# Performance work log

Hardware: AMD Instinct MI355X
Metric: run time of the kernel (lower is better)

## Reference

```python
import jax, jax.numpy as jnp
import numpy as np
from jax import lax

N, C, H, W = 64, 96, 18, 32
S_IN = 320          # input_state_size
HEADS, HD = 4, 96 // 4
HID = 96            # HIDDEN_SIZE
ENC = 320           # ENC_SIZE
K = 3               # KERNEL_SIZE


def _conv(x, k, b):
    y = lax.conv_general_dilated(x, k, (1, 1), 'SAME',
                                 dimension_numbers=('NCHW', 'OIHW', 'NCHW'))
    return y + b[None, :, None, None]


def setup_inputs() -> dict:
    key = jax.random.key(0)
    ks = jax.random.split(key, 16)
    sc = 0.02
    inp = {
        'x': jax.random.normal(ks[0], (N, C, H, W), jnp.float32),
        'x_state': jax.random.normal(ks[1], (N, S_IN), jnp.float32),
        'actor_keys': jax.random.randint(ks[2], (N,), 0, N),
        'hidden_states': 0.1 * jax.random.normal(ks[3], (N, HID, H, W), jnp.float32),
        # modulation Linear(S_IN -> 2*C), bias init 0
        'W_mod': sc * jax.random.normal(ks[4], (S_IN, 2 * C), jnp.float32),
        'b_mod': jnp.zeros((2 * C,), jnp.float32),
        # FiLM attention: qkv 1x1 proj and output proj
        'W_qkv': sc * jax.random.normal(ks[5], (C, 3 * C), jnp.float32),
        'b_qkv': jnp.zeros((3 * C,), jnp.float32),
        'W_proj': sc * jax.random.normal(ks[6], (C, C), jnp.float32),
        'b_proj': jnp.zeros((C,), jnp.float32),
        # IRConv2dCell (ConvGRU-style): gates conv (2C -> 2*HID), candidate conv (2C -> HID)
        'K_zr': sc * jax.random.normal(ks[7], (2 * HID, 2 * C, K, K), jnp.float32),
        'b_zr': jnp.zeros((2 * HID,), jnp.float32),
        'K_c': sc * jax.random.normal(ks[8], (HID, 2 * C, K, K), jnp.float32),
        'b_c': jnp.zeros((HID,), jnp.float32),
        # PosConv: learned positional map + 1x1 conv to ENC
        'pos_emb': sc * jax.random.normal(ks[9], (1, HID, H, W), jnp.float32),
        'W_pos': sc * jax.random.normal(ks[10], (ENC, HID), jnp.float32),
        'b_pos': jnp.zeros((ENC,), jnp.float32),
    }
    return inp


def reference(x, x_state, actor_keys, hidden_states,
              W_mod, b_mod, W_qkv, b_qkv, W_proj, b_proj,
              K_zr, b_zr, K_c, b_c, pos_emb, W_pos, b_pos):
    HW = H * W
    # modulation -> FiLM params
    mod = x_state @ W_mod + b_mod                       # [N, 2C]
    mm, mb = jnp.split(mod, 2, axis=1)                  # [N, C] each
    # FiLM-conditioned attention over spatial positions
    xm = x * mm[:, :, None, None] + mb[:, :, None, None]  # [N,C,H,W]
    xf = xm.reshape(N, C, HW).transpose(0, 2, 1)          # [N,HW,C]
    qkv = xf @ W_qkv + b_qkv                              # [N,HW,3C]
    q, k, v = jnp.split(qkv, 3, axis=-1)
    q = q.reshape(N, HW, HEADS, HD).transpose(0, 2, 1, 3)  # [N,h,HW,hd]
    k = k.reshape(N, HW, HEADS, HD).transpose(0, 2, 1, 3)
    v = v.reshape(N, HW, HEADS, HD).transpose(0, 2, 1, 3)
    attn = jax.nn.softmax(jnp.einsum('nhqd,nhkd->nhqk', q, k) / np.sqrt(HD), axis=-1)
    o = jnp.einsum('nhqk,nhkd->nhqd', attn, v)            # [N,h,HW,hd]
    o = o.transpose(0, 2, 1, 3).reshape(N, HW, C)
    o = o @ W_proj + b_proj
    y = x + o.transpose(0, 2, 1).reshape(N, C, H, W)      # residual
    # actor-keyed recurrent conv memory cell (gather per actor key)
    h = hidden_states[actor_keys]                         # [N,HID,H,W]
    xh = jnp.concatenate([y, h], axis=1)                  # [N,2C,H,W]
    zr = _conv(xh, K_zr, b_zr)
    z, r = jnp.split(jax.nn.sigmoid(zr), 2, axis=1)
    c = jnp.tanh(_conv(jnp.concatenate([y, r * h], axis=1), K_c, b_c))
    h_new = (1.0 - z) * h + z * c                         # [N,HID,H,W]
    # pooled outputs
    x_visual = h_new.reshape(N, HID, H // 2, 2, W // 2, 2).mean(axis=(3, 5))
    e = h_new + pos_emb
    enc = jnp.einsum('nchw,oc->nohw', e, W_pos) + b_pos[None, :, None, None]
    x_visual_enc = enc.max(axis=(2, 3))                   # [N,ENC]
    return (x_visual, x_visual_enc)
```

## Files before the change

kernel.cpp:

```cpp
#include <hip/hip_runtime.h>
#include <hip/hip_bf16.h>
#include <math.h>

#define NN 64
#define CC 96
#define HH 18
#define WW 32
#define HWP 576
#define SIN 320
#define NHEADS 4
#define HDIM 24
#define HIDC 96
#define ENCC 320

#define MOD_OFF   0
#define A_OFF     12288
#define Y_OFF     (A_OFF)
#define Z_OFF     (A_OFF + 3538944)
#define RH_OFF    (A_OFF + 7077888)
#define O_OFF     (A_OFF + 10616832)
#define HN_OFF    (O_OFF)
#define PART_OFF  (O_OFF + 3538944)
#define WTZR_OFF  (PART_OFF + 163840)
#define WTC_OFF   (WTZR_OFF + 165888)

typedef __attribute__((ext_vector_type(8))) short short8;
typedef __attribute__((ext_vector_type(4))) float f32x4;
typedef __attribute__((ext_vector_type(2))) unsigned int uint2v;
#define MFMA16(a, b, c) __builtin_amdgcn_mfma_f32_16x16x32_bf16(a, b, c, 0, 0, 0)

__device__ inline unsigned short f2bf(float f) {
  __hip_bfloat16 h = __float2bfloat16(f);
  return *reinterpret_cast<unsigned short*>(&h);
}
__device__ inline unsigned int cvtpk(float lo, float hi) {
  unsigned int r;
  asm volatile("v_cvt_pk_bf16_f32 %0, %1, %2" : "=v"(r) : "v"(lo), "v"(hi));
  return r;
}
union S8U { short8 s; unsigned int u[4]; };

__global__ __launch_bounds__(192) void k_mod(const float* __restrict__ xs,
    const float* __restrict__ Wm, const float* __restrict__ bm,
    float* __restrict__ mod) {
  __shared__ float s[SIN];
  int n = blockIdx.x;
  for (int i = threadIdx.x; i < SIN; i += 192) s[i] = xs[n * SIN + i];
  __syncthreads();
  int j = threadIdx.x;
  float acc = bm[j];
  #pragma unroll 4
  for (int k = 0; k < SIN; ++k) acc = fmaf(s[k], Wm[k * 192 + j], acc);
  mod[n * 192 + j] = acc;
}

__global__ __launch_bounds__(256) void k_qkv(const float* __restrict__ x,
    const float* __restrict__ mod, const float* __restrict__ Wq,
    const float* __restrict__ bq, float* __restrict__ qkv) {
  int id = blockIdx.x;
  int n = id & 63, pt = id >> 6;
  int p0 = pt * 96;
  __shared__ __align__(16) short XT[96 * 104];
  int tid = threadIdx.x, lane = tid & 63, wid = tid >> 6;
  int wr = wid >> 1, wcn = wid & 1;
  int cl = lane & 15, kg = lane >> 4;
  #pragma unroll
  for (int w = 0; w < 9; ++w) {
    int lin = tid + 256 * w;
    int cp = lin / 48, pp = (lin % 48) * 2;
    float mA = mod[n * 192 + 2 * cp], bA = mod[n * 192 + 96 + 2 * cp];
    float mB = mod[n * 192 + 2 * cp + 1], bB = mod[n * 192 + 96 + 2 * cp + 1];
    float2 xa = *reinterpret_cast<const float2*>(
        &x[((size_t)n * CC + 2 * cp) * HWP + p0 + pp]);
    float2 xb = *reinterpret_cast<const float2*>(
        &x[((size_t)n * CC + 2 * cp + 1) * HWP + p0 + pp]);
    *reinterpret_cast<unsigned int*>(&XT[pp * 104 + 2 * cp]) =
        cvtpk(fmaf(xa.x, mA, bA), fmaf(xb.x, mB, bB));
    *reinterpret_cast<unsigned int*>(&XT[(pp + 1) * 104 + 2 * cp]) =
        cvtpk(fmaf(xa.y, mA, bA), fmaf(xb.y, mB, bB));
  }
  __syncthreads();

  f32x4 acc[3][9];
  #pragma unroll
  for (int mt = 0; mt < 3; ++mt)
    #pragma unroll
    for (int nt = 0; nt < 9; ++nt) acc[mt][nt] = (f32x4){0.f, 0.f, 0.f, 0.f};

  #pragma unroll
  for (int kc = 0; kc < 3; ++kc) {
    short8 af[3];
    #pragma unroll
    for (int mt = 0; mt < 3; ++mt) {
      int row = wr * 48 + mt * 16 + cl;
      af[mt] = *reinterpret_cast<const short8*>(
          &XT[row * 104 + kc * 32 + kg * 8]);
    }
    #pragma unroll
    for (int nt = 0; nt < 9; ++nt) {
      int j = wcn * 144 + nt * 16 + cl;
      const float* wp = Wq + (size_t)(kc * 32 + kg * 8) * 288 + j;
      S8U b;
      b.u[0] = cvtpk(wp[0], wp[288]);
      b.u[1] = cvtpk(wp[576], wp[864]);
      b.u[2] = cvtpk(wp[1152], wp[1440]);
      b.u[3] = cvtpk(wp[1728], wp[2016]);
      #pragma unroll
      for (int mt = 0; mt < 3; ++mt)
        acc[mt][nt] = MFMA16(af[mt], b.s, acc[mt][nt]);
    }
  }

  #pragma unroll
  for (int nt = 0; nt < 9; ++nt) {
    int j = wcn * 144 + nt * 16 + cl;
    float bias = bq[j];
    #pragma unroll
    for (int mt = 0; mt < 3; ++mt) {
      int pr = p0 + wr * 48 + mt * 16 + kg * 4;
      float* dst = qkv + ((size_t)n * HWP + pr) * 288 + j;
      dst[0] = acc[mt][nt][0] + bias;
      dst[288] = acc[mt][nt][1] + bias;
      dst[576] = acc[mt][nt][2] + bias;
      dst[864] = acc[mt][nt][3] + bias;
    }
  }
}

__global__ __launch_bounds__(256) void k_attn(const float* __restrict__ qkv,
                                              float* __restrict__ o) {
  int id = blockIdx.x;
  int n = id & 63, head = id >> 6;
  __shared__ __align__(16) short K_lds[576 * 40];
  __shared__ __align__(16) short VT_lds[24 * 584];
  __shared__ __align__(16) short P_lds[4 * 144 * 40];
  int tid = threadIdx.x, lane = tid & 63, wid = tid >> 6;
  int cl = lane & 15, kg = lane >> 4;
  const float* base = qkv + (size_t)n * HWP * 288;
  int qoff = head * HDIM, koff = CC + head * HDIM, voff = 2 * CC + head * HDIM;
  const float scale = 0.2041241452319315f;

  for (int p = tid; p < HWP; p += 256) {
    const float* ksrc = base + (size_t)p * 288 + koff;
    #pragma unroll
    for (int g = 0; g < 3; ++g) {
      float4 a = *(const float4*)(ksrc + g * 8);
      float4 b = *(const float4*)(ksrc + g * 8 + 4);
      S8U t;
      t.u[0] = cvtpk(a.x, a.y); t.u[1] = cvtpk(a.z, a.w);
      t.u[2] = cvtpk(b.x, b.y); t.u[3] = cvtpk(b.z, b.w);
      *reinterpret_cast<short8*>(&K_lds[p * 40 + g * 8]) = t.s;
    }
    *reinterpret_cast<short8*>(&K_lds[p * 40 + 24]) =
        (short8){0, 0, 0, 0, 0, 0, 0, 0};
    const float* vsrc = base + (size_t)p * 288 + voff;
    #pragma unroll
    for (int d = 0; d < HDIM; ++d) VT_lds[d * 584 + p] = (short)f2bf(vsrc[d]);
  }

  int qbase = wid * 144;
  short8 qf[9];
  #pragma unroll
  for (int qt = 0; qt < 9; ++qt) {
    if (kg < 3) {
      const float* qs =
          base + (size_t)(qbase + qt * 16 + cl) * 288 + qoff + kg * 8;
      float4 a = *(const float4*)qs;
      float4 b = *(const float4*)(qs + 4);
      S8U t;
      t.u[0] = cvtpk(a.x * scale, a.y * scale);
      t.u[1] = cvtpk(a.z * scale, a.w * scale);
      t.u[2] = cvtpk(b.x * scale, b.y * scale);
      t.u[3] = cvtpk(b.z * scale, b.w * scale);
      qf[qt] = t.s;
    } else {
      qf[qt] = (short8){0, 0, 0, 0, 0, 0, 0, 0};
    }
  }
  __syncthreads();

  f32x4 acc[9][2];
  float m[9], l[9];
  #pragma unroll
  for (int qt = 0; qt < 9; ++qt) {
    acc[qt][0] = (f32x4){0.f, 0.f, 0.f, 0.f};
    acc[qt][1] = (f32x4){0.f, 0.f, 0.f, 0.f};
    m[qt] = -1e30f; l[qt] = 0.f;
  }
  short* pw = P_lds + wid * 5760;
  const f32x4 z4 = (f32x4){0.f, 0.f, 0.f, 0.f};

  for (int ch = 0; ch < 18; ++ch) {
    int key0 = ch * 32;
    short8 ka0 = *reinterpret_cast<const short8*>(
        &K_lds[(key0 + cl) * 40 + kg * 8]);
    short8 ka1 = *reinterpret_cast<const short8*>(
        &K_lds[(key0 + 16 + cl) * 40 + kg * 8]);
    #pragma unroll
    for (int qt = 0; qt < 9; ++qt) {
      f32x4 s0 = MFMA16(ka0, qf[qt], z4);
      f32x4 s1 = MFMA16(ka1, qf[qt], z4);
      float mx = fmaxf(fmaxf(fmaxf(s0[0], s0[1]), fmaxf(s0[2], s0[3])),
                       fmaxf(fmaxf(s1[0], s1[1]), fmaxf(s1[2], s1[3])));
      mx = fmaxf(mx, __shfl_xor(mx, 16));
      mx = fmaxf(mx, __shfl_xor(mx, 32));
      float mn = fmaxf(m[qt], mx);
      float corr = __expf(m[qt] - mn);
      float p0 = __expf(s0[0] - mn), p1 = __expf(s0[1] - mn);
      float p2 = __expf(s0[2] - mn), p3 = __expf(s0[3] - mn);
      float p4 = __expf(s1[0] - mn), p5 = __expf(s1[1] - mn);
      float p6 = __expf(s1[2] - mn), p7 = __expf(s1[3] - mn);
      float sum = ((p0 + p1) + (p2 + p3)) + ((p4 + p5) + (p6 + p7));
      sum += __shfl_xor(sum, 16);
      sum += __shfl_xor(sum, 32);
      l[qt] = l[qt] * corr + sum;
      m[qt] = mn;
      float c0 = __shfl(corr, kg * 4 + 0);
      float c1 = __shfl(corr, kg * 4 + 1);
      float c2 = __shfl(corr, kg * 4 + 2);
      float c3 = __shfl(corr, kg * 4 + 3);
      acc[qt][0][0] *= c0; acc[qt][0][1] *= c1;
      acc[qt][0][2] *= c2; acc[qt][0][3] *= c3;
      acc[qt][1][0] *= c0; acc[qt][1][1] *= c1;
      acc[qt][1][2] *= c2; acc[qt][1][3] *= c3;
      uint2v w0 = {cvtpk(p0, p1), cvtpk(p2, p3)};
      uint2v w1 = {cvtpk(p4, p5), cvtpk(p6, p7)};
      short* prow = pw + (qt * 16 + cl) * 40;
      *reinterpret_cast<uint2v*>(&prow[4 * kg]) = w0;
      *reinterpret_cast<uint2v*>(&prow[16 + 4 * kg]) = w1;
    }
    short8 vb0 = *reinterpret_cast<const short8*>(
        &VT_lds[cl * 584 + key0 + kg * 8]);
    short8 vb1 = (cl < 8) ? *reinterpret_cast<const short8*>(
                                &VT_lds[(16 + cl) * 584 + key0 + kg * 8])
                          : (short8){0, 0, 0, 0, 0, 0, 0, 0};
    #pragma unroll
    for (int qt = 0; qt < 9; ++qt) {
      short8 pa = *reinterpret_cast<const short8*>(
          &pw[(qt * 16 + cl) * 40 + kg * 8]);
      acc[qt][0] = MFMA16(pa, vb0, acc[qt][0]);
      acc[qt][1] = MFMA16(pa, vb1, acc[qt][1]);
    }
  }

  #pragma unroll
  for (int qt = 0; qt < 9; ++qt) {
    float li0 = 1.f / __shfl(l[qt], kg * 4 + 0);
    float li1 = 1.f / __shfl(l[qt], kg * 4 + 1);
    float li2 = 1.f / __shfl(l[qt], kg * 4 + 2);
    float li3 = 1.f / __shfl(l[qt], kg * 4 + 3);
    #pragma unroll
    for (int dt = 0; dt < 2; ++dt) {
      int d = dt * 16 + cl;
      if (dt == 1 && cl >= 8) continue;
      size_t ob = ((size_t)n * HWP + qbase + qt * 16 + kg * 4) * CC
                  + head * HDIM + d;
      o[ob] = acc[qt][dt][0] * li0;
      o[ob + CC] = acc[qt][dt][1] * li1;
      o[ob + 2 * CC] = acc[qt][dt][2] * li2;
      o[ob + 3 * CC] = acc[qt][dt][3] * li3;
    }
  }
}

__global__ __launch_bounds__(256) void k_proj(const float* __restrict__ o,
    const float* __restrict__ Wp, const float* __restrict__ bp,
    const float* __restrict__ x, float* __restrict__ y) {
  int id = blockIdx.x;
  int n = id & 63, pt = id >> 6;
  int p0 = pt * 96;
  __shared__ __align__(16) short XT[96 * 104];
  int tid = threadIdx.x, lane = tid & 63, wid = tid >> 6;
  int wr = wid >> 1, wcn = wid & 1;
  int cl = lane & 15, kg = lane >> 4;
  #pragma unroll
  for (int w = 0; w < 9; ++w) {
    int lin = tid + 256 * w;
    int p = lin / 24, cg = lin % 24;
    float4 v = *reinterpret_cast<const float4*>(
        &o[((size_t)n * HWP + p0 + p) * CC + cg * 4]);
    uint2v u = {cvtpk(v.x, v.y), cvtpk(v.z, v.w)};
    *reinterpret_cast<uint2v*>(&XT[p * 104 + cg * 4]) = u;
  }
  __syncthreads();

  f32x4 acc[3][3];
  #pragma unroll
  for (int mt = 0; mt < 3; ++mt)
    #pragma unroll
    for (int nt = 0; nt < 3; ++nt) acc[mt][nt] = (f32x4){0.f, 0.f, 0.f, 0.f};

  #pragma unroll
  for (int kc = 0; kc < 3; ++kc) {
    short8 af[3];
    #pragma unroll
    for (int mt = 0; mt < 3; ++mt) {
      int row = wr * 48 + mt * 16 + cl;
      af[mt] = *reinterpret_cast<const short8*>(
          &XT[row * 104 + kc * 32 + kg * 8]);
    }
    #pragma unroll
    for (int nt = 0; nt < 3; ++nt) {
      int j = wcn * 48 + nt * 16 + cl;
      const float* wp = Wp + (size_t)(kc * 32 + kg * 8) * 96 + j;
      S8U b;
      b.u[0] = cvtpk(wp[0], wp[96]);
      b.u[1] = cvtpk(wp[192], wp[288]);
      b.u[2] = cvtpk(wp[384], wp[480]);
      b.u[3] = cvtpk(wp[576], wp[672]);
      #pragma unroll
      for (int mt = 0; mt < 3; ++mt)
        acc[mt][nt] = MFMA16(af[mt], b.s, acc[mt][nt]);
    }
  }

  #pragma unroll
  for (int nt = 0; nt < 3; ++nt) {
    int j = wcn * 48 + nt * 16 + cl;
    float bias = bp[j];
    #pragma unroll
    for (int mt = 0; mt < 3; ++mt) {
      int pr = p0 + wr * 48 + mt * 16 + kg * 4;
      size_t yi = ((size_t)n * CC + j) * HWP + pr;
      float4 xv = *reinterpret_cast<const float4*>(&x[yi]);
      float4 o4 = {xv.x + acc[mt][nt][0] + bias, xv.y + acc[mt][nt][1] + bias,
                   xv.z + acc[mt][nt][2] + bias, xv.w + acc[mt][nt][3] + bias};
      *reinterpret_cast<float4*>(&y[yi]) = o4;
    }
  }
}

__global__ __launch_bounds__(256) void k_wt(const float* __restrict__ Kzr,
    const float* __restrict__ Kc, short* __restrict__ wz,
    short* __restrict__ wc) {
  int idx = blockIdx.x * 256 + threadIdx.x;
  if (idx < 36864) {
    int oc = idx / 192, ic = idx % 192;
    const float* s = Kzr + (size_t)idx * 9;
    #pragma unroll
    for (int t = 0; t < 9; ++t)
      wz[(t * 192 + oc) * 192 + ic] = (short)f2bf(s[t]);
  } else {
    int j = idx - 36864;
    if (j < 18432) {
      int oc = j / 192, ic = j % 192;
      const float* s = Kc + (size_t)j * 9;
      #pragma unroll
      for (int t = 0; t < 9; ++t)
        wc[(t * 96 + oc) * 192 + ic] = (short)f2bf(s[t]);
    }
  }
}


#define CONV_LD(CI, A, B, SRC2)                                              \
  {                                                                          \
    const float* s0_ = ((CI) < 3)                                            \
        ? y + ((size_t)n * CC + (CI) * 32 + 2 * icp) * HWP                   \
        : (SRC2);                                                            \
    const float* s1_ = s0_ + HWP;                                            \
    _Pragma("unroll")                                                        \
    for (int j = 0; j < 5; ++j) {                                            \
      int pg = pg0 + pb + 2 * j;                                             \
      bool ok = (pg >= 0 && pg < HWP);                                       \
      A[j] = ok ? *reinterpret_cast<const float2*>(s0_ + pg)                 \
                : float2{0.f, 0.f};                                          \
      B[j] = ok ? *reinterpret_cast<const float2*>(s1_ + pg)                 \
                : float2{0.f, 0.f};                                          \
    }                                                                        \
  }

#define CONV_ST(XB, A, B)                                                    \
  {                                                                          \
    _Pragma("unroll")                                                        \
    for (int j = 0; j < 5; ++j) {                                            \
      int pos_ = pb + 2 * j;                                                 \
      int pidx_ = (pos_ >> 5) * 34 + 1 + (pos_ & 31);                        \
      int uc0_ = (icp + 4 * ((pidx_ >> 5) & 3)) & 15;                        \
      int uc1_ = (icp + 4 * (((pidx_ + 1) >> 5) & 3)) & 15;                  \
      *reinterpret_cast<unsigned int*>((XB) + pidx_ * 40 + 2 * uc0_) =       \
          (unsigned int)f2bf(A[j].x) | ((unsigned int)f2bf(B[j].x) << 16);   \
      *reinterpret_cast<unsigned int*>((XB) + (pidx_ + 1) * 40 + 2 * uc1_) = \
          (unsigned int)f2bf(A[j].y) | ((unsigned int)f2bf(B[j].y) << 16);   \
    }                                                                        \
  }

__global__ __launch_bounds__(256, 4) void k_conv_zr(const float* __restrict__ y,
    const float* __restrict__ hidden, const int* __restrict__ keys,
    const short* __restrict__ wt, const float* __restrict__ bb,
    float* __restrict__ z, float* __restrict__ rh) {
  int id = blockIdx.x;
  int n = id & 63, b = id >> 6;
  int bp = b % 6, bo = b / 6;
  int key = keys[n];
  int ocb = bo * 96;
  __shared__ short XT[2][6800];
  int tid = threadIdx.x;
  int lane = tid & 63, wid = tid >> 6;
  int wr = wid >> 1, wc = wid & 1;
  int col = lane & 15, kg = lane >> 4;
  int icp = tid >> 4, psub = tid & 15;
  int pb = psub * 10;
  int pg0 = (3 * bp - 1) * 32;

  for (int i = tid; i < 6800; i += 256) reinterpret_cast<int*>(XT)[i] = 0;

  f32x4 acc[3][3];
  #pragma unroll
  for (int m = 0; m < 3; ++m)
    #pragma unroll
    for (int nt = 0; nt < 3; ++nt) acc[m][nt] = (f32x4){0.f, 0.f, 0.f, 0.f};
  int rowm[3], pxm[3];
  #pragma unroll
  for (int m = 0; m < 3; ++m) {
    int pl = wr * 48 + m * 16 + col;
    rowm[m] = pl >> 5;
    pxm[m] = pl & 31;
  }
  int wl = (ocb + wc * 48 + col) * 192 + kg * 8;
  const float* hsrc = hidden + (size_t)key * HIDC * HWP;
  __syncthreads();

  float2 A0[5], B0[5], A1[5], B1[5];
  CONV_LD(0, A0, B0, hsrc)

  #define ZR_STEP(CI, AIN, BIN, AOUT, BOUT)                                  \
    {                                                                        \
      short* Xb = &XT[(CI) & 1][0];                                          \
      if ((CI) < 5)                                                          \
        CONV_LD((CI) + 1, AOUT, BOUT,                                        \
                hsrc + (size_t)(((CI) - 2) * 32 + 2 * icp) * HWP)            \
      CONV_ST(Xb, AIN, BIN)                                                  \
      __syncthreads();                                                       \
      const short* wci = wt + wl + (CI) * 32;                                \
      _Pragma("unroll")                                                      \
      for (int t = 0; t < 9; ++t) {                                          \
        short8 b0 = *reinterpret_cast<const short8*>(wci + t * 36864);       \
        short8 b1 = *reinterpret_cast<const short8*>(wci + t * 36864 + 3072);\
        short8 b2 = *reinterpret_cast<const short8*>(wci + t * 36864 + 6144);\
        int dyp = t / 3, dxp = t % 3;                                        \
        _Pragma("unroll")                                                    \
        for (int m = 0; m < 3; ++m) {                                        \
          int pidx_ = (rowm[m] + dyp) * 34 + pxm[m] + dxp;                   \
          int so_ = pidx_ * 40 + (((kg + (pidx_ >> 5)) & 3) << 3);           \
          short8 a = *reinterpret_cast<const short8*>(Xb + so_);             \
          acc[m][0] = MFMA16(a, b0, acc[m][0]);                              \
          acc[m][1] = MFMA16(a, b1, acc[m][1]);                              \
          acc[m][2] = MFMA16(a, b2, acc[m][2]);                              \
        }                                                                    \
      }                                                                      \
    }

  ZR_STEP(0, A0, B0, A1, B1)
  ZR_STEP(1, A1, B1, A0, B0)
  ZR_STEP(2, A0, B0, A1, B1)
  ZR_STEP(3, A1, B1, A0, B0)
  ZR_STEP(4, A0, B0, A1, B1)
  ZR_STEP(5, A1, B1, A0, B0)
  #undef ZR_STEP

  #pragma unroll
  for (int nt = 0; nt < 3; ++nt) {
    int oc = ocb + wc * 48 + nt * 16 + col;
    float bias = bb[oc];
    #pragma unroll
    for (int m = 0; m < 3; ++m) {
      int p0 = bp * 96 + wr * 48 + m * 16 + kg * 4;
      f32x4 v = acc[m][nt];
      float e0 = 1.f / (1.f + __expf(-(v[0] + bias)));
      float e1 = 1.f / (1.f + __expf(-(v[1] + bias)));
      float e2 = 1.f / (1.f + __expf(-(v[2] + bias)));
      float e3 = 1.f / (1.f + __expf(-(v[3] + bias)));
      if (oc < CC) {
        float4 o4 = {e0, e1, e2, e3};
        *reinterpret_cast<float4*>(&z[((size_t)n * CC + oc) * HWP + p0]) = o4;
      } else {
        int c2 = oc - CC;
        float4 h4 = *reinterpret_cast<const float4*>(
            &hidden[((size_t)key * HIDC + c2) * HWP + p0]);
        float4 o4 = {e0 * h4.x, e1 * h4.y, e2 * h4.z, e3 * h4.w};
        *reinterpret_cast<float4*>(&rh[((size_t)n * CC + c2) * HWP + p0]) = o4;
      }
    }
  }
}

__global__ __launch_bounds__(256) void k_conv_c(const float* __restrict__ y,
    const float* __restrict__ rh, const int* __restrict__ keys,
    const float* __restrict__ z, const float* __restrict__ hidden,
    const short* __restrict__ wt, const float* __restrict__ bb,
    float* __restrict__ hn) {
  int id = blockIdx.x;
  int n = id & 63, bp = id >> 6;
  int key = keys[n];
  __shared__ short XT[2][6800];
  int tid = threadIdx.x;
  int lane = tid & 63, wid = tid >> 6;
  int wr = wid >> 1, wc = wid & 1;
  int col = lane & 15, kg = lane >> 4;
  int icp = tid >> 4, psub = tid & 15;
  int pb = psub * 10;
  int pg0 = (3 * bp - 1) * 32;

  for (int i = tid; i < 6800; i += 256) reinterpret_cast<int*>(XT)[i] = 0;

  f32x4 acc[3][3];
  #pragma unroll
  for (int m = 0; m < 3; ++m)
    #pragma unroll
    for (int nt = 0; nt < 3; ++nt) acc[m][nt] = (f32x4){0.f, 0.f, 0.f, 0.f};
  int rowm[3], pxm[3];
  #pragma unroll
  for (int m = 0; m < 3; ++m) {
    int pl = wr * 48 + m * 16 + col;
    rowm[m] = pl >> 5;
    pxm[m] = pl & 31;
  }
  int wl = (wc * 48 + col) * 192 + kg * 8;
  const float* rsrc = rh + (size_t)n * CC * HWP + (size_t)2 * icp * HWP;
  __syncthreads();

  float2 A0[5], B0[5], A1[5], B1[5];
  CONV_LD(0, A0, B0, rsrc)

  #define C_STEP(CI, AIN, BIN, AOUT, BOUT)                                   \
    {                                                                        \
      short* Xb = &XT[(CI) & 1][0];                                          \
      if ((CI) < 5)                                                          \
        CONV_LD((CI) + 1, AOUT, BOUT,                                        \
                rsrc + (size_t)(((CI) - 2) * 32) * HWP)                      \
      CONV_ST(Xb, AIN, BIN)                                                  \
      __syncthreads();                                                       \
      const short* wci = wt + wl + (CI) * 32;                                \
      _Pragma("unroll")                                                      \
      for (int t = 0; t < 9; ++t) {                                          \
        short8 b0 = *reinterpret_cast<const short8*>(wci + t * 18432);       \
        short8 b1 = *reinterpret_cast<const short8*>(wci + t * 18432 + 3072);\
        short8 b2 = *reinterpret_cast<const short8*>(wci + t * 18432 + 6144);\
        int dyp = t / 3, dxp = t % 3;                                        \
        _Pragma("unroll")                                                    \
        for (int m = 0; m < 3; ++m) {                                        \
          int pidx_ = (rowm[m] + dyp) * 34 + pxm[m] + dxp;                   \
          int so_ = pidx_ * 40 + (((kg + (pidx_ >> 5)) & 3) << 3);           \
          short8 a = *reinterpret_cast<const short8*>(Xb + so_);             \
          acc[m][0] = MFMA16(a, b0, acc[m][0]);                              \
          acc[m][1] = MFMA16(a, b1, acc[m][1]);                              \
          acc[m][2] = MFMA16(a, b2, acc[m][2]);                              \
        }                                                                    \
      }                                                                      \
    }

  C_STEP(0, A0, B0, A1, B1)
  C_STEP(1, A1, B1, A0, B0)
  C_STEP(2, A0, B0, A1, B1)
  C_STEP(3, A1, B1, A0, B0)
  C_STEP(4, A0, B0, A1, B1)
  C_STEP(5, A1, B1, A0, B0)
  #undef C_STEP

  #pragma unroll
  for (int nt = 0; nt < 3; ++nt) {
    int oc = wc * 48 + nt * 16 + col;
    float bias = bb[oc];
    #pragma unroll
    for (int m = 0; m < 3; ++m) {
      int p0 = bp * 96 + wr * 48 + m * 16 + kg * 4;
      f32x4 v = acc[m][nt];
      float c0 = tanhf(v[0] + bias);
      float c1 = tanhf(v[1] + bias);
      float c2v = tanhf(v[2] + bias);
      float c3 = tanhf(v[3] + bias);
      float4 z4 = *reinterpret_cast<const float4*>(
          &z[((size_t)n * CC + oc) * HWP + p0]);
      float4 h4 = *reinterpret_cast<const float4*>(
          &hidden[((size_t)key * HIDC + oc) * HWP + p0]);
      float4 o4 = {(1.f - z4.x) * h4.x + z4.x * c0,
                   (1.f - z4.y) * h4.y + z4.y * c1,
                   (1.f - z4.z) * h4.z + z4.z * c2v,
                   (1.f - z4.w) * h4.w + z4.w * c3};
      *reinterpret_cast<float4*>(&hn[((size_t)n * CC + oc) * HWP + p0]) = o4;
    }
  }
}

__global__ void k_pool(const float* __restrict__ hn, float* __restrict__ out) {
  int idx = blockIdx.x * 256 + threadIdx.x;
  if (idx >= NN * CC * 9 * 16) return;
  int j = idx & 15, i = (idx >> 4) % 9, nc = idx / 144;
  const float* b = hn + (size_t)nc * HWP + (2 * i) * WW + 2 * j;
  out[idx] = 0.25f * (b[0] + b[1] + b[WW] + b[WW + 1]);
}

__global__ __launch_bounds__(256) void k_enc(const float* __restrict__ hn,
    const float* __restrict__ pos, const float* __restrict__ Wp,
    float* __restrict__ part) {
  int id = blockIdx.x;
  int n = id & 63, pt = id >> 6;
  int p0 = pt * 96;
  __shared__ __align__(16) short XT[96 * 104];
  int tid = threadIdx.x, lane = tid & 63, wid = tid >> 6;
  int wr = wid >> 1, wcn = wid & 1;
  int cl = lane & 15, kg = lane >> 4;
  #pragma unroll
  for (int w = 0; w < 9; ++w) {
    int lin = tid + 256 * w;
    int cp = lin / 48, pp = (lin % 48) * 2;
    float2 ha = *reinterpret_cast<const float2*>(
        &hn[((size_t)n * CC + 2 * cp) * HWP + p0 + pp]);
    float2 hb = *reinterpret_cast<const float2*>(
        &hn[((size_t)n * CC + 2 * cp + 1) * HWP + p0 + pp]);
    float2 pa = *reinterpret_cast<const float2*>(&pos[(2 * cp) * HWP + p0 + pp]);
    float2 pc = *reinterpret_cast<const float2*>(
        &pos[(2 * cp + 1) * HWP + p0 + pp]);
    *reinterpret_cast<unsigned int*>(&XT[pp * 104 + 2 * cp]) =
        cvtpk(ha.x + pa.x, hb.x + pc.x);
    *reinterpret_cast<unsigned int*>(&XT[(pp + 1) * 104 + 2 * cp]) =
        cvtpk(ha.y + pa.y, hb.y + pc.y);
  }
  __syncthreads();

  f32x4 acc[3][10];
  #pragma unroll
  for (int mt = 0; mt < 3; ++mt)
    #pragma unroll
    for (int nt = 0; nt < 10; ++nt) acc[mt][nt] = (f32x4){0.f, 0.f, 0.f, 0.f};

  #pragma unroll
  for (int kc = 0; kc < 3; ++kc) {
    short8 af[3];
    #pragma unroll
    for (int mt = 0; mt < 3; ++mt) {
      int row = wr * 48 + mt * 16 + cl;
      af[mt] = *reinterpret_cast<const short8*>(
          &XT[row * 104 + kc * 32 + kg * 8]);
    }
    #pragma unroll
    for (int nt = 0; nt < 10; ++nt) {
      int oc = wcn * 160 + nt * 16 + cl;
      const float* wp = Wp + (size_t)oc * CC + kc * 32 + kg * 8;
      float4 w0 = *reinterpret_cast<const float4*>(wp);
      float4 w1 = *reinterpret_cast<const float4*>(wp + 4);
      S8U b;
      b.u[0] = cvtpk(w0.x, w0.y); b.u[1] = cvtpk(w0.z, w0.w);
      b.u[2] = cvtpk(w1.x, w1.y); b.u[3] = cvtpk(w1.z, w1.w);
      #pragma unroll
      for (int mt = 0; mt < 3; ++mt)
        acc[mt][nt] = MFMA16(af[mt], b.s, acc[mt][nt]);
    }
  }

  #pragma unroll
  for (int nt = 0; nt < 10; ++nt) {
    float mx = -1e30f;
    #pragma unroll
    for (int mt = 0; mt < 3; ++mt) {
      mx = fmaxf(mx, fmaxf(fmaxf(acc[mt][nt][0], acc[mt][nt][1]),
                           fmaxf(acc[mt][nt][2], acc[mt][nt][3])));
    }
    mx = fmaxf(mx, __shfl_xor(mx, 16));
    mx = fmaxf(mx, __shfl_xor(mx, 32));
    if (kg == 0) {
      int oc = wcn * 160 + nt * 16 + cl;
      part[(((size_t)n * 6 + pt) * 2 + wr) * ENCC + oc] = mx;
    }
  }
}

__global__ __launch_bounds__(320) void k_reduce(const float* __restrict__ part,
    const float* __restrict__ bpos, float* __restrict__ out) {
  int n = blockIdx.x, o = threadIdx.x;
  float mx = -1e30f;
  #pragma unroll
  for (int t = 0; t < 12; ++t)
    mx = fmaxf(mx, part[((size_t)n * 12 + t) * ENCC + o]);
  out[NN * CC * 144 + n * ENCC + o] = mx + bpos[o];
}

extern "C" void kernel_launch(void* const* d_in, const int* in_sizes, int n_in,
                              void* d_out, int out_size, void* d_ws, size_t ws_size,
                              hipStream_t stream) {
  const float* x       = (const float*)d_in[0];
  const float* x_state = (const float*)d_in[1];
  const int*   keys    = (const int*)d_in[2];
  const float* hidden  = (const float*)d_in[3];
  const float* W_mod   = (const float*)d_in[4];
  const float* b_mod   = (const float*)d_in[5];
  const float* W_qkv   = (const float*)d_in[6];
  const float* b_qkv   = (const float*)d_in[7];
  const float* W_proj  = (const float*)d_in[8];
  const float* b_proj  = (const float*)d_in[9];
  const float* K_zr    = (const float*)d_in[10];
  const float* b_zr    = (const float*)d_in[11];
  const float* K_c     = (const float*)d_in[12];
  const float* b_c     = (const float*)d_in[13];
  const float* pos_emb = (const float*)d_in[14];
  const float* W_pos   = (const float*)d_in[15];
  const float* b_pos   = (const float*)d_in[16];
  float* out = (float*)d_out;
  float* ws  = (float*)d_ws;
  short* wtzr = (short*)(ws + WTZR_OFF);
  short* wtc  = (short*)(ws + WTC_OFF);

  k_wt<<<216, 256, 0, stream>>>(K_zr, K_c, wtzr, wtc);
  k_mod<<<NN, 192, 0, stream>>>(x_state, W_mod, b_mod, ws + MOD_OFF);
  k_qkv<<<384, 256, 0, stream>>>(x, ws + MOD_OFF, W_qkv, b_qkv, ws + A_OFF);
  k_attn<<<256, 256, 0, stream>>>(ws + A_OFF, ws + O_OFF);
  k_proj<<<384, 256, 0, stream>>>(ws + O_OFF, W_proj, b_proj, x, ws + Y_OFF);
  k_conv_zr<<<768, 256, 0, stream>>>(ws + Y_OFF, hidden, keys, wtzr, b_zr,
                                     ws + Z_OFF, ws + RH_OFF);
  k_conv_c<<<384, 256, 0, stream>>>(ws + Y_OFF, ws + RH_OFF, keys, ws + Z_OFF,
                                    hidden, wtc, b_c, ws + HN_OFF);
  k_pool<<<3456, 256, 0, stream>>>(ws + HN_OFF, out);
  k_enc<<<384, 256, 0, stream>>>(ws + HN_OFF, pos_emb, W_pos, ws + PART_OFF);
  k_reduce<<<NN, 320, 0, stream>>>(ws + PART_OFF, b_pos, out);
}
```

Measured before the change: 314.9 us.

## Stage full input tile in LDS once and loop taps outside channels in GRU convs

Both conv kernels now load all 192 input channels of the halo tile into one large padded LDS buffer with a single barrier, instead of double-buffering 32-channel chunks with a barrier per chunk. The MFMA loop becomes tap-outer and channel-inner, and the padded row stride of 200 replaces the XOR-style swizzle. This removes per-chunk synchronisation and lets global loads issue all at once. In exchange LDS use grows to about 68 KB per block, which cuts occupancy, and the launch-bounds occupancy hint is dropped. There is also no overlap left between the global loads and the MFMA work.

```diff
diff --git a/kernel.cpp b/kernel.cpp
--- a/kernel.cpp
+++ b/kernel.cpp
@@ -353,39 +353,7 @@
 }
 
 
-#define CONV_LD(CI, A, B, SRC2)                                              \
-  {                                                                          \
-    const float* s0_ = ((CI) < 3)                                            \
-        ? y + ((size_t)n * CC + (CI) * 32 + 2 * icp) * HWP                   \
-        : (SRC2);                                                            \
-    const float* s1_ = s0_ + HWP;                                            \
-    _Pragma("unroll")                                                        \
-    for (int j = 0; j < 5; ++j) {                                            \
-      int pg = pg0 + pb + 2 * j;                                             \
-      bool ok = (pg >= 0 && pg < HWP);                                       \
-      A[j] = ok ? *reinterpret_cast<const float2*>(s0_ + pg)                 \
-                : float2{0.f, 0.f};                                          \
-      B[j] = ok ? *reinterpret_cast<const float2*>(s1_ + pg)                 \
-                : float2{0.f, 0.f};                                          \
-    }                                                                        \
-  }
-
-#define CONV_ST(XB, A, B)                                                    \
-  {                                                                          \
-    _Pragma("unroll")                                                        \
-    for (int j = 0; j < 5; ++j) {                                            \
-      int pos_ = pb + 2 * j;                                                 \
-      int pidx_ = (pos_ >> 5) * 34 + 1 + (pos_ & 31);                        \
-      int uc0_ = (icp + 4 * ((pidx_ >> 5) & 3)) & 15;                        \
-      int uc1_ = (icp + 4 * (((pidx_ + 1) >> 5) & 3)) & 15;                  \
-      *reinterpret_cast<unsigned int*>((XB) + pidx_ * 40 + 2 * uc0_) =       \
-          (unsigned int)f2bf(A[j].x) | ((unsigned int)f2bf(B[j].x) << 16);   \
-      *reinterpret_cast<unsigned int*>((XB) + (pidx_ + 1) * 40 + 2 * uc1_) = \
-          (unsigned int)f2bf(A[j].y) | ((unsigned int)f2bf(B[j].y) << 16);   \
-    }                                                                        \
-  }
-
-__global__ __launch_bounds__(256, 4) void k_conv_zr(const float* __restrict__ y,
+__global__ __launch_bounds__(256) void k_conv_zr(const float* __restrict__ y,
     const float* __restrict__ hidden, const int* __restrict__ keys,
     const short* __restrict__ wt, const float* __restrict__ bb,
     float* __restrict__ z, float* __restrict__ rh) {
@@ -394,7 +362,7 @@
   int bp = b % 6, bo = b / 6;
   int key = keys[n];
   int ocb = bo * 96;
-  __shared__ short XT[2][6800];
+  __shared__ __align__(16) short XT[170 * 200];
   int tid = threadIdx.x;
   int lane = tid & 63, wid = tid >> 6;
   int wr = wid >> 1, wc = wid & 1;
@@ -402,8 +370,9 @@
   int icp = tid >> 4, psub = tid & 15;
   int pb = psub * 10;
   int pg0 = (3 * bp - 1) * 32;
-
-  for (int i = tid; i < 6800; i += 256) reinterpret_cast<int*>(XT)[i] = 0;
+  unsigned int* XTu = reinterpret_cast<unsigned int*>(XT);
+
+  for (int i = tid; i < 17000; i += 256) XTu[i] = 0;
 
   f32x4 acc[3][3];
   #pragma unroll
@@ -421,43 +390,48 @@
   const float* hsrc = hidden + (size_t)key * HIDC * HWP;
   __syncthreads();
 
-  float2 A0[5], B0[5], A1[5], B1[5];
-  CONV_LD(0, A0, B0, hsrc)
-
-  #define ZR_STEP(CI, AIN, BIN, AOUT, BOUT)                                  \
-    {                                                                        \
-      short* Xb = &XT[(CI) & 1][0];                                          \
-      if ((CI) < 5)                                                          \
-        CONV_LD((CI) + 1, AOUT, BOUT,                                        \
-                hsrc + (size_t)(((CI) - 2) * 32 + 2 * icp) * HWP)            \
-      CONV_ST(Xb, AIN, BIN)                                                  \
-      __syncthreads();                                                       \
-      const short* wci = wt + wl + (CI) * 32;                                \
-      _Pragma("unroll")                                                      \
-      for (int t = 0; t < 9; ++t) {                                          \
-        short8 b0 = *reinterpret_cast<const short8*>(wci + t * 36864);       \
-        short8 b1 = *reinterpret_cast<const short8*>(wci + t * 36864 + 3072);\
-        short8 b2 = *reinterpret_cast<const short8*>(wci + t * 36864 + 6144);\
-        int dyp = t / 3, dxp = t % 3;                                        \
-        _Pragma("unroll")                                                    \
-        for (int m = 0; m < 3; ++m) {                                        \
-          int pidx_ = (rowm[m] + dyp) * 34 + pxm[m] + dxp;                   \
-          int so_ = pidx_ * 40 + (((kg + (pidx_ >> 5)) & 3) << 3);           \
-          short8 a = *reinterpret_cast<const short8*>(Xb + so_);             \
-          acc[m][0] = MFMA16(a, b0, acc[m][0]);                              \
-          acc[m][1] = MFMA16(a, b1, acc[m][1]);                              \
-          acc[m][2] = MFMA16(a, b2, acc[m][2]);                              \
-        }                                                                    \
-      }                                                                      \
-    }
-
-  ZR_STEP(0, A0, B0, A1, B1)
-  ZR_STEP(1, A1, B1, A0, B0)
-  ZR_STEP(2, A0, B0, A1, B1)
-  ZR_STEP(3, A1, B1, A0, B0)
-  ZR_STEP(4, A0, B0, A1, B1)
-  ZR_STEP(5, A1, B1, A0, B0)
-  #undef ZR_STEP
+  #pragma unroll
+  for (int c = 0; c < 6; ++c) {
+    const float* s0 = (c < 3)
+        ? y + ((size_t)n * CC + c * 32 + 2 * icp) * HWP
+        : hsrc + (size_t)((c - 3) * 32 + 2 * icp) * HWP;
+    const float* s1 = s0 + HWP;
+    #pragma unroll
+    for (int j = 0; j < 5; ++j) {
+      int pos = pb + 2 * j;
+      int pg = pg0 + pos;
+      bool ok = (pg >= 0 && pg < HWP);
+      float2 a = ok ? *reinterpret_cast<const float2*>(s0 + pg)
+                    : float2{0.f, 0.f};
+      float2 bv = ok ? *reinterpret_cast<const float2*>(s1 + pg)
+                     : float2{0.f, 0.f};
+      int pidx0 = (pos >> 5) * 34 + 1 + (pos & 31);
+      int pidx1 = ((pos + 1) >> 5) * 34 + 1 + ((pos + 1) & 31);
+      XTu[pidx0 * 100 + c * 16 + icp] = cvtpk(a.x, bv.x);
+      XTu[pidx1 * 100 + c * 16 + icp] = cvtpk(a.y, bv.y);
+    }
+  }
+  __syncthreads();
+
+  for (int t = 0; t < 9; ++t) {
+    int dyp = t / 3, dxp = t % 3;
+    const short* wci = wt + wl + t * 36864;
+    #pragma unroll
+    for (int q = 0; q < 6; ++q) {
+      short8 b0 = *reinterpret_cast<const short8*>(wci + q * 32);
+      short8 b1 = *reinterpret_cast<const short8*>(wci + q * 32 + 3072);
+      short8 b2 = *reinterpret_cast<const short8*>(wci + q * 32 + 6144);
+      #pragma unroll
+      for (int m = 0; m < 3; ++m) {
+        int pidx = (rowm[m] + dyp) * 34 + pxm[m] + dxp;
+        short8 a = *reinterpret_cast<const short8*>(
+            XT + pidx * 200 + q * 32 + kg * 8);
+        acc[m][0] = MFMA16(a, b0, acc[m][0]);
+        acc[m][1] = MFMA16(a, b1, acc[m][1]);
+        acc[m][2] = MFMA16(a, b2, acc[m][2]);
+      }
+    }
+  }
 
   #pragma unroll
   for (int nt = 0; nt < 3; ++nt) {
@@ -493,7 +467,7 @@
   int id = blockIdx.x;
   int n = id & 63, bp = id >> 6;
   int key = keys[n];
-  __shared__ short XT[2][6800];
+  __shared__ __align__(16) short XT[170 * 200];
   int tid = threadIdx.x;
   int lane = tid & 63, wid = tid >> 6;
   int wr = wid >> 1, wc = wid & 1;
@@ -501,8 +475,9 @@
   int icp = tid >> 4, psub = tid & 15;
   int pb = psub * 10;
   int pg0 = (3 * bp - 1) * 32;
-
-  for (int i = tid; i < 6800; i += 256) reinterpret_cast<int*>(XT)[i] = 0;
+  unsigned int* XTu = reinterpret_cast<unsigned int*>(XT);
+
+  for (int i = tid; i < 17000; i += 256) XTu[i] = 0;
 
   f32x4 acc[3][3];
   #pragma unroll
@@ -517,46 +492,51 @@
     pxm[m] = pl & 31;
   }
   int wl = (wc * 48 + col) * 192 + kg * 8;
-  const float* rsrc = rh + (size_t)n * CC * HWP + (size_t)2 * icp * HWP;
-  __syncthreads();
-
-  float2 A0[5], B0[5], A1[5], B1[5];
-  CONV_LD(0, A0, B0, rsrc)
-
-  #define C_STEP(CI, AIN, BIN, AOUT, BOUT)                                   \
-    {                                                                        \
-      short* Xb = &XT[(CI) & 1][0];                                          \
-      if ((CI) < 5)                                                          \
-        CONV_LD((CI) + 1, AOUT, BOUT,                                        \
-                rsrc + (size_t)(((CI) - 2) * 32) * HWP)                      \
-      CONV_ST(Xb, AIN, BIN)                                                  \
-      __syncthreads();                                                       \
-      const short* wci = wt + wl + (CI) * 32;                                \
-      _Pragma("unroll")                                                      \
-      for (int t = 0; t < 9; ++t) {                                          \
-        short8 b0 = *reinterpret_cast<const short8*>(wci + t * 18432);       \
-        short8 b1 = *reinterpret_cast<const short8*>(wci + t * 18432 + 3072);\
-        short8 b2 = *reinterpret_cast<const short8*>(wci + t * 18432 + 6144);\
-        int dyp = t / 3, dxp = t % 3;                                        \
-        _Pragma("unroll")                                                    \
-        for (int m = 0; m < 3; ++m) {                                        \
-          int pidx_ = (rowm[m] + dyp) * 34 + pxm[m] + dxp;                   \
-          int so_ = pidx_ * 40 + (((kg + (pidx_ >> 5)) & 3) << 3);           \
-          short8 a = *reinterpret_cast<const short8*>(Xb + so_);             \
-          acc[m][0] = MFMA16(a, b0, acc[m][0]);                              \
-          acc[m][1] = MFMA16(a, b1, acc[m][1]);                              \
-          acc[m][2] = MFMA16(a, b2, acc[m][2]);                              \
-        }                                                                    \
-      }                                                                      \
-    }
-
-  C_STEP(0, A0, B0, A1, B1)
-  C_STEP(1, A1, B1, A0, B0)
-  C_STEP(2, A0, B0, A1, B1)
-  C_STEP(3, A1, B1, A0, B0)
-  C_STEP(4, A0, B0, A1, B1)
-  C_STEP(5, A1, B1, A0, B0)
-  #undef C_STEP
+  const float* rsrc = rh + (size_t)n * CC * HWP;
+  __syncthreads();
+
+  #pragma unroll
+  for (int c = 0; c < 6; ++c) {
+    const float* s0 = (c < 3)
+        ? y + ((size_t)n * CC + c * 32 + 2 * icp) * HWP
+        : rsrc + (size_t)((c - 3) * 32 + 2 * icp) * HWP;
+    const float* s1 = s0 + HWP;
+    #pragma unroll
+    for (int j = 0; j < 5; ++j) {
+      int pos = pb + 2 * j;
+      int pg = pg0 + pos;
+      bool ok = (pg >= 0 && pg < HWP);
+      float2 a = ok ? *reinterpret_cast<const float2*>(s0 + pg)
+                    : float2{0.f, 0.f};
+      float2 bv = ok ? *reinterpret_cast<const float2*>(s1 + pg)
+                     : float2{0.f, 0.f};
+      int pidx0 = (pos >> 5) * 34 + 1 + (pos & 31);
+      int pidx1 = ((pos + 1) >> 5) * 34 + 1 + ((pos + 1) & 31);
+      XTu[pidx0 * 100 + c * 16 + icp] = cvtpk(a.x, bv.x);
+      XTu[pidx1 * 100 + c * 16 + icp] = cvtpk(a.y, bv.y);
+    }
+  }
+  __syncthreads();
+
+  for (int t = 0; t < 9; ++t) {
+    int dyp = t / 3, dxp = t % 3;
+    const short* wci = wt + wl + t * 18432;
+    #pragma unroll
+    for (int q = 0; q < 6; ++q) {
+      short8 b0 = *reinterpret_cast<const short8*>(wci + q * 32);
+      short8 b1 = *reinterpret_cast<const short8*>(wci + q * 32 + 3072);
+      short8 b2 = *reinterpret_cast<const short8*>(wci + q * 32 + 6144);
+      #pragma unroll
+      for (int m = 0; m < 3; ++m) {
+        int pidx = (rowm[m] + dyp) * 34 + pxm[m] + dxp;
+        short8 a = *reinterpret_cast<const short8*>(
+            XT + pidx * 200 + q * 32 + kg * 8);
+        acc[m][0] = MFMA16(a, b0, acc[m][0]);
+        acc[m][1] = MFMA16(a, b1, acc[m][1]);
+        acc[m][2] = MFMA16(a, b2, acc[m][2]);
+      }
+    }
+  }
 
   #pragma unroll
   for (int nt = 0; nt < 3; ++nt) {
```

New measurement: 314.8 us. Within noise of the previous version (-0.0%).
